# Kernel optimization log

Hardware: AMD Instinct MI355X
Metric: run time of the kernel (lower is better)

## Reference

```python
import jax, jax.numpy as jnp
import numpy as np

B, N, M = 2, 2048, 1024
C, CTX, H = 1024, 1024, 16
D = C // H
HID = int(C * 4.0)
EPS = 1e-6


def _ln(h):
    # LayerNorm32: fp32 layernorm, eps=1e-6, no affine params
    h32 = h.astype(jnp.float32)
    mu = jnp.mean(h32, axis=-1, keepdims=True)
    var = jnp.var(h32, axis=-1, keepdims=True)
    return ((h32 - mu) * jax.lax.rsqrt(var + EPS)).astype(h.dtype)


def _sdpa(q, k, v):
    # q: [B,Q,H,D], k/v: [B,K,H,D]
    scale = 1.0 / np.sqrt(D)
    s = jnp.einsum('bqhd,bkhd->bhqk', q, k) * scale
    p = jax.nn.softmax(s, axis=-1)
    return jnp.einsum('bhqk,bkhd->bqhd', p, v)


def _forward(x, context, Wqkv, bqkv, Wos, bos, Wq, bq, Wkv, bkv, Woc, boc, W1, b1, W2, b2):
    Bx, Nx, _ = x.shape
    Mx = context.shape[1]
    # --- self-attention (attn_mode='full') ---
    h = _ln(x)
    qkv = (h @ Wqkv + bqkv).reshape(Bx, Nx, 3, H, D)
    q, k, v = qkv[:, :, 0], qkv[:, :, 1], qkv[:, :, 2]
    a = _sdpa(q, k, v).reshape(Bx, Nx, C)
    x = x + (a @ Wos + bos)
    # --- cross-attention (always 'full') ---
    h = _ln(x)
    q = (h @ Wq + bq).reshape(Bx, Nx, H, D)
    kv = (context @ Wkv + bkv).reshape(Bx, Mx, 2, H, D)
    k, v = kv[:, :, 0], kv[:, :, 1]
    a = _sdpa(q, k, v).reshape(Bx, Nx, C)
    x = x + (a @ Woc + boc)
    # --- FFN with tanh-approx GELU ---
    h = _ln(x)
    x = x + (jax.nn.gelu(h @ W1 + b1, approximate=True) @ W2 + b2)
    return x


def setup_inputs() -> dict:
    key = jax.random.key(0)
    ks = jax.random.split(key, 12)
    rn = lambda k, shape: (jax.random.normal(k, shape, jnp.float32) * 0.02)
    return {
        'x': jax.random.normal(ks[0], (B, N, C), jnp.float32),
        'context': jax.random.normal(ks[1], (B, M, CTX), jnp.float32),
        'Wqkv': rn(ks[2], (C, 3 * C)), 'bqkv': jnp.zeros((3 * C,), jnp.float32),
        'Wos': rn(ks[3], (C, C)), 'bos': jnp.zeros((C,), jnp.float32),
        'Wq': rn(ks[4], (C, C)), 'bq': jnp.zeros((C,), jnp.float32),
        'Wkv': rn(ks[5], (CTX, 2 * C)), 'bkv': jnp.zeros((2 * C,), jnp.float32),
        'Woc': rn(ks[6], (C, C)), 'boc': jnp.zeros((C,), jnp.float32),
        'W1': rn(ks[7], (C, HID)), 'b1': jnp.zeros((HID,), jnp.float32),
        'W2': rn(ks[8], (HID, C)), 'b2': jnp.zeros((C,), jnp.float32),
    }


def reference(x, context, Wqkv, bqkv, Wos, bos, Wq, bq, Wkv, bkv, Woc, boc, W1, b1, W2, b2):
    return _forward(x, context, Wqkv, bqkv, Wos, bos, Wq, bq, Wkv, bkv, Woc, boc, W1, b1, W2, b2)
```

## Files before the change

### kernel.cpp

```cpp
#include <hip/hip_runtime.h>
#include <cstdint>

typedef unsigned short u16;
typedef short bf16x8 __attribute__((ext_vector_type(8)));
typedef unsigned short u16x8 __attribute__((ext_vector_type(8)));
typedef float f32x4 __attribute__((ext_vector_type(4)));

__device__ __forceinline__ u16 f2bf(float f) {
  union { float f; uint32_t u; } v; v.f = f;
  uint32_t r = (v.u + 0x7fffu + ((v.u >> 16) & 1u)) >> 16;
  return (u16)r;
}

__device__ __forceinline__ void gload_lds16(const u16* g, u16* l) {
  __builtin_amdgcn_global_load_lds(
      (const __attribute__((address_space(1))) void*)g,
      (__attribute__((address_space(3))) void*)l, 16, 0, 0);
}

__device__ __forceinline__ void ln_body(const float* __restrict__ x,
                                        u16* __restrict__ h, int row) {
  const int tid = threadIdx.x;
  const float4 v = *reinterpret_cast<const float4*>(x + (long)row * 1024 + tid * 4);
  float s  = v.x + v.y + v.z + v.w;
  float ss = v.x * v.x + v.y * v.y + v.z * v.z + v.w * v.w;
#pragma unroll
  for (int off = 32; off >= 1; off >>= 1) {
    s  += __shfl_xor(s, off, 64);
    ss += __shfl_xor(ss, off, 64);
  }
  __shared__ float red[8];
  const int wave = tid >> 6, lane = tid & 63;
  if (lane == 0) { red[wave] = s; red[4 + wave] = ss; }
  __syncthreads();
  s  = red[0] + red[1] + red[2] + red[3];
  ss = red[4] + red[5] + red[6] + red[7];
  const float mu   = s * (1.0f / 1024.0f);
  const float var  = ss * (1.0f / 1024.0f) - mu * mu;
  const float rstd = rsqrtf(var + 1e-6f);
  ushort4 o;
  o.x = f2bf((v.x - mu) * rstd);
  o.y = f2bf((v.y - mu) * rstd);
  o.z = f2bf((v.z - mu) * rstd);
  o.w = f2bf((v.w - mu) * rstd);
  *reinterpret_cast<ushort4*>(h + (long)row * 1024 + tid * 4) = o;
}

__global__ __launch_bounds__(256) void ln_kernel(const float* __restrict__ x,
                                                 u16* __restrict__ h) {
  ln_body(x, h, blockIdx.x);
}

struct WEnt { const float* W; u16* Wt; int K, N, tEnd; };
struct WEnts { WEnt e[4]; int n; };

__device__ __forceinline__ void wconv_body(const WEnts& args, int t) {
  __shared__ u16 tile[64][72];
  int i = 0, tStart = 0;
  while (i < args.n - 1 && t >= args.e[i].tEnd) { tStart = args.e[i].tEnd; i++; }
  const float* W = args.e[i].W;
  u16* Wt = args.e[i].Wt;
  const int K = args.e[i].K, N = args.e[i].N;
  const int rel = t - tStart;
  const int ntn = N >> 6;
  const int tn = rel % ntn, tk = rel / ntn;
  const int n0 = tn * 64, k0 = tk * 64;

  const int th = threadIdx.x;
  const int c4 = (th & 15) * 4;
  const int r  = th >> 4;
#pragma unroll
  for (int ii = 0; ii < 4; ii++) {
    const int row = ii * 16 + r;
    const float4 v = *reinterpret_cast<const float4*>(W + (long)(k0 + row) * N + n0 + c4);
    tile[c4 + 0][row] = f2bf(v.x);
    tile[c4 + 1][row] = f2bf(v.y);
    tile[c4 + 2][row] = f2bf(v.z);
    tile[c4 + 3][row] = f2bf(v.w);
  }
  __syncthreads();
  const int c8 = (th & 7) * 8;
  const int rn = th >> 3;
#pragma unroll
  for (int ii = 0; ii < 2; ii++) {
    const int row = ii * 32 + rn;
    *reinterpret_cast<u16x8*>(Wt + (long)(n0 + row) * K + k0 + c8) =
        *reinterpret_cast<const u16x8*>(&tile[row][c8]);
  }
}

__global__ __launch_bounds__(256) void wconvert_all(WEnts args) {
  wconv_body(args, blockIdx.x);
}

__global__ __launch_bounds__(256) void ln_wconv_combo(const float* __restrict__ x,
                                                      u16* __restrict__ h, int nLn,
                                                      WEnts args) {
  if ((int)blockIdx.x < nLn) ln_body(x, h, blockIdx.x);
  else                       wconv_body(args, blockIdx.x - nLn);
}

__global__ __launch_bounds__(256) void wconv_f2bf_combo(WEnts args, int nW,
                                                        const float* __restrict__ in,
                                                        u16* __restrict__ out) {
  if ((int)blockIdx.x < nW) {
    wconv_body(args, blockIdx.x);
  } else {
    const long i = ((long)(blockIdx.x - nW) * 256 + threadIdx.x) * 4;
    const float4 v = *reinterpret_cast<const float4*>(in + i);
    ushort4 o;
    o.x = f2bf(v.x); o.y = f2bf(v.y); o.z = f2bf(v.z); o.w = f2bf(v.w);
    *reinterpret_cast<ushort4*>(out + i) = o;
  }
}

__global__ __launch_bounds__(256) void vtrans(const u16* __restrict__ V,
                                              u16* __restrict__ Vt,
                                              int vStride, long vBatch, int nk) {
  __shared__ u16 tile[64][72];
  const int t = threadIdx.x;
  const int b = blockIdx.z, h = blockIdx.y, n0 = blockIdx.x * 64;
  const u16* vp = V + (long)b * vBatch + h * 64;
  u16* op = Vt + (long)(b * 16 + h) * 64 * (long)nk + n0;
  const int ch = t & 7;
#pragma unroll
  for (int i = 0; i < 2; i++) {
    const int n = (t >> 3) + i * 32;
    const u16x8 v = *reinterpret_cast<const u16x8*>(vp + (long)(n0 + n) * vStride + ch * 8);
#pragma unroll
    for (int j = 0; j < 8; j++) tile[ch * 8 + j][n] = v[j];
  }
  __syncthreads();
#pragma unroll
  for (int i = 0; i < 2; i++) {
    const int d = (t >> 3) + i * 32;
    *reinterpret_cast<u16x8*>(op + (long)d * nk + ch * 8) =
        *reinterpret_cast<const u16x8*>(&tile[d][ch * 8]);
  }
}

template <int TN, bool OUT_BF16, bool GELU_ACT, bool RES>
__device__ __forceinline__ void gemm_core(
    const u16* __restrict__ A, const u16* __restrict__ Bt,
    const float* __restrict__ bias, const float* __restrict__ res,
    void* __restrict__ Cout, int Ndim, int Kdim, int m0, int n0,
    u16* Al, u16* Bl, int qcols, float qscale) {
  constexpr int NF = TN / 32;
  constexpr int ABUF = 128 * 64;
  constexpr int BBUF = TN * 64;
  const int tid  = threadIdx.x;
  const int lane = tid & 63, wave = tid >> 6;
  const int quad = lane >> 4, l15 = lane & 15;
  const int wr = wave >> 1, wc = wave & 1;

  f32x4 acc[4][NF];
  const f32x4 vzero = {0.f, 0.f, 0.f, 0.f};
#pragma unroll
  for (int i = 0; i < 4; i++)
#pragma unroll
    for (int jj = 0; jj < NF; jj++) acc[i][jj] = vzero;

  const int srcRow = lane >> 3;
  const int srcG   = ((lane & 7) ^ (srcRow & 7)) * 8;
  const u16* gA = A  + (long)(m0 + srcRow) * Kdim + srcG;
  const u16* gB = Bt + (long)(n0 + srcRow) * Kdim + srcG;

  auto stage = [&](int k0, int p) {
#pragma unroll
    for (int i = 0; i < 4; i++)
      gload_lds16(gA + (long)(wave * 32 + i * 8) * Kdim + k0,
                  Al + p * ABUF + wave * 2048 + i * 512);
#pragma unroll
    for (int i = 0; i < TN / 32; i++)
      gload_lds16(gB + (long)(wave * (TN / 4) + i * 8) * Kdim + k0,
                  Bl + p * BBUF + wave * (TN * 16) + i * 512);
  };

  const int off0 = (quad ^ (l15 & 7)) * 8;

  stage(0, 0);
  int p = 0;
  for (int k0 = 0; k0 < Kdim; k0 += 64, p ^= 1) {
    __syncthreads();
    bf16x8 af[2][4], bfr[2][NF];
    const u16* ab = Al + p * ABUF;
    const u16* bb = Bl + p * BBUF;
#pragma unroll
    for (int mt = 0; mt < 4; mt++) {
      const int r = (wr * 64 + mt * 16 + l15) * 64;
      af[0][mt] = *reinterpret_cast<const bf16x8*>(ab + r + off0);
      af[1][mt] = *reinterpret_cast<const bf16x8*>(ab + r + (off0 ^ 32));
    }
#pragma unroll
    for (int nt = 0; nt < NF; nt++) {
      const int r = (wc * (NF * 16) + nt * 16 + l15) * 64;
      bfr[0][nt] = *reinterpret_cast<const bf16x8*>(bb + r + off0);
      bfr[1][nt] = *reinterpret_cast<const bf16x8*>(bb + r + (off0 ^ 32));
    }
    if (k0 + 64 < Kdim) stage(k0 + 64, p ^ 1);
#pragma unroll
    for (int s = 0; s < 2; s++)
#pragma unroll
      for (int mt = 0; mt < 4; mt++)
#pragma unroll
        for (int nt = 0; nt < NF; nt++)
          acc[mt][nt] = __builtin_amdgcn_mfma_f32_16x16x32_bf16(af[s][mt], bfr[s][nt], acc[mt][nt], 0, 0, 0);
  }

#pragma unroll
  for (int nt = 0; nt < NF; nt++) {
    const int col = n0 + wc * (NF * 16) + nt * 16 + l15;
    const float bv = bias[col];
    const float cs = (col < qcols) ? qscale : 1.0f;
#pragma unroll
    for (int mt = 0; mt < 4; mt++) {
#pragma unroll
      for (int r = 0; r < 4; r++) {
        const int row = m0 + wr * 64 + mt * 16 + quad * 4 + r;
        float y = (acc[mt][nt][r] + bv) * cs;
        if (GELU_ACT) {
          const float t = 0.7978845608028654f * (y + 0.044715f * y * y * y);
          y = y / (1.0f + __builtin_amdgcn_exp2f(-2.885390081777927f * t));
        }
        if (RES) y += res[(long)row * Ndim + col];
        if (OUT_BF16)
          ((u16*)Cout)[(long)row * Ndim + col] = f2bf(y);
        else
          ((float*)Cout)[(long)row * Ndim + col] = y;
      }
    }
  }
}

template <int TN, int SX, bool OUT_BF16, bool GELU_ACT, bool RES>
__global__ __launch_bounds__(256, 2) void gemm_bt(
    const u16* __restrict__ A, const u16* __restrict__ Bt,
    const float* __restrict__ bias, const float* __restrict__ res,
    void* __restrict__ Cout, int Ndim, int Kdim, int lx, int ly,
    int qcols, float qscale) {
  __shared__ u16 Al[2 * 128 * 64];
  __shared__ u16 Bl[2 * TN * 64];
  const int j = blockIdx.x;
  const int c = j & 7, kk = j >> 3;
  const int cx = c % SX, cy = c / SX;
  const int bx = cx * lx + (kk % lx);
  const int by = cy * ly + (kk / lx);
  gemm_core<TN, OUT_BF16, GELU_ACT, RES>(
      A, Bt, bias, res, Cout, Ndim, Kdim, by * 128, bx * TN, Al, Bl, qcols, qscale);
}

struct GemmSeg {
  const u16* A; const u16* Bt; const float* bias; u16* C;
  int Ndim, Kdim, SX, lx, ly, qcols; float qscale;
};
struct GemmDualP { GemmSeg s0, s1; int nBlk0; };

template <int TN>
__global__ __launch_bounds__(256, 2) void gemm_dual(GemmDualP pp) {
  __shared__ u16 Al[2 * 128 * 64];
  __shared__ u16 Bl[2 * TN * 64];
  int j = blockIdx.x;
  GemmSeg s;
  if (j < pp.nBlk0) { s = pp.s0; } else { s = pp.s1; j -= pp.nBlk0; }
  const int c = j & 7, kk = j >> 3;
  const int cx = c % s.SX, cy = c / s.SX;
  const int bx = cx * s.lx + (kk % s.lx);
  const int by = cy * s.ly + (kk / s.lx);
  gemm_core<TN, true, false, false>(
      s.A, s.Bt, s.bias, nullptr, s.C, s.Ndim, s.Kdim, by * 128, bx * TN, Al, Bl,
      s.qcols, s.qscale);
}

__global__ __launch_bounds__(256, 2) void attn_kernel(
    const u16* __restrict__ Q, const u16* __restrict__ K, const u16* __restrict__ Vt,
    u16* __restrict__ O, int nk, int qStride, int kStride, int oStride,
    long qBatch, long kBatch, long oBatch) {
  __shared__ u16 Kt[2][2 * 64 * 64];
  __shared__ u16 Vl[2][2 * 64 * 64];
  __shared__ u16 Pl[4][32 * 64];

  const int tid = threadIdx.x;
  const int lane = tid & 63, wave = tid >> 6;
  const int quad = lane >> 4, l15 = lane & 15;

  const int j = blockIdx.x;
  const int xcd = j & 7, slot = j >> 3;
  const int g = xcd * 4 + (slot >> 4);
  const int qt = slot & 15;
  const int hh = g & 15, b = g >> 4;

  const u16* qp = Q + (long)b * qBatch + hh * 64;
  const u16* kp = K + (long)b * kBatch + hh * 64;
  const u16* vp = Vt + (long)(b * 16 + hh) * 64 * (long)nk;

  bf16x8 qf[2][2];
  const int qrow = qt * 128 + wave * 32 + l15;
#pragma unroll
  for (int qg = 0; qg < 2; qg++) {
    qf[qg][0] = *reinterpret_cast<const bf16x8*>(qp + (long)(qrow + qg * 16) * qStride + quad * 8);
    qf[qg][1] = *reinterpret_cast<const bf16x8*>(qp + (long)(qrow + qg * 16) * qStride + 32 + quad * 8);
  }

  const int r8 = lane >> 3;
  const int gcol = ((lane & 7) ^ r8) * 8;
  const u16* kgA = kp + (long)(wave * 8 + r8) * kStride + gcol;
  const u16* kgB = kp + (long)((wave + 4) * 8 + r8) * kStride + gcol;
  const u16* vgA = vp + (long)(wave * 8 + r8) * nk + gcol;
  const u16* vgB = vp + (long)((wave + 4) * 8 + r8) * nk + gcol;

  const int cF = (quad ^ (l15 & 7)) * 8;

  const f32x4 vzero = {0.f, 0.f, 0.f, 0.f};
  const bf16x8 vones = {16256, 16256, 16256, 16256, 16256, 16256, 16256, 16256};
  f32x4 oAcc[2][4];
  f32x4 lAcc[2];
#pragma unroll
  for (int qg = 0; qg < 2; qg++) {
    lAcc[qg] = vzero;
#pragma unroll
    for (int i = 0; i < 4; i++) oAcc[qg][i] = vzero;
  }

  const int nWin = nk >> 7;
  const long kAdv = (long)128 * kStride;

  auto stage = [&](int w, int p) {
#pragma unroll
    for (int h2 = 0; h2 < 2; h2++) {
      const long kOff = w * kAdv + (long)(h2 * 64) * kStride;
      gload_lds16(kgA + kOff, &Kt[p][h2 * 4096 + wave * 512]);
      gload_lds16(kgB + kOff, &Kt[p][h2 * 4096 + (wave + 4) * 512]);
      const int vOff = w * 128 + h2 * 64;
      gload_lds16(vgA + vOff, &Vl[p][h2 * 4096 + wave * 512]);
      gload_lds16(vgB + vOff, &Vl[p][h2 * 4096 + (wave + 4) * 512]);
    }
  };

  stage(0, 0);
  int p = 0;
  for (int w = 0; w < nWin; w++, p ^= 1) {
    __syncthreads();
    if (w + 1 < nWin) stage(w + 1, p ^ 1);

#pragma unroll
    for (int h2 = 0; h2 < 2; h2++) {
      const u16* Kh = &Kt[p][h2 * 4096];
      const u16* Vh = &Vl[p][h2 * 4096];

      f32x4 st[2][4];
      __builtin_amdgcn_s_setprio(1);
#pragma unroll
      for (int mt = 0; mt < 4; mt++) {
        const bf16x8 kf0 = *reinterpret_cast<const bf16x8*>(&Kh[(mt * 16 + l15) * 64 + cF]);
        const bf16x8 kf1 = *reinterpret_cast<const bf16x8*>(&Kh[(mt * 16 + l15) * 64 + (cF ^ 32)]);
#pragma unroll
        for (int qg = 0; qg < 2; qg++) {
          f32x4 z = vzero;
          z = __builtin_amdgcn_mfma_f32_16x16x32_bf16(kf0, qf[qg][0], z, 0, 0, 0);
          z = __builtin_amdgcn_mfma_f32_16x16x32_bf16(kf1, qf[qg][1], z, 0, 0, 0);
          st[qg][mt] = z;
        }
      }
      __builtin_amdgcn_s_setprio(0);

#pragma unroll
      for (int qg = 0; qg < 2; qg++) {
        u16* plw = &Pl[wave][(qg * 16 + l15) * 64];
#pragma unroll
        for (int mt = 0; mt < 4; mt++) {
          const float e0 = __builtin_amdgcn_exp2f(st[qg][mt][0]);
          const float e1 = __builtin_amdgcn_exp2f(st[qg][mt][1]);
          const float e2 = __builtin_amdgcn_exp2f(st[qg][mt][2]);
          const float e3 = __builtin_amdgcn_exp2f(st[qg][mt][3]);
          uint2 w2;
          asm("v_cvt_pk_bf16_f32 %0, %1, %2" : "=v"(w2.x) : "v"(e0), "v"(e1));
          asm("v_cvt_pk_bf16_f32 %0, %1, %2" : "=v"(w2.y) : "v"(e2), "v"(e3));
          const int pcol = (((mt * 2 + (quad >> 1)) ^ (l15 & 7)) * 8) + (quad & 1) * 4;
          *reinterpret_cast<uint2*>(&plw[pcol]) = w2;
        }
      }

      bf16x8 pf[2][2];
#pragma unroll
      for (int qg = 0; qg < 2; qg++) {
        const u16* plw = &Pl[wave][(qg * 16 + l15) * 64];
        pf[qg][0] = *reinterpret_cast<const bf16x8*>(&plw[cF]);
        pf[qg][1] = *reinterpret_cast<const bf16x8*>(&plw[cF ^ 32]);
        lAcc[qg] = __builtin_amdgcn_mfma_f32_16x16x32_bf16(pf[qg][0], vones, lAcc[qg], 0, 0, 0);
        lAcc[qg] = __builtin_amdgcn_mfma_f32_16x16x32_bf16(pf[qg][1], vones, lAcc[qg], 0, 0, 0);
      }
      __builtin_amdgcn_s_setprio(1);
#pragma unroll
      for (int dt = 0; dt < 4; dt++) {
        const bf16x8 vf0 = *reinterpret_cast<const bf16x8*>(&Vh[(dt * 16 + l15) * 64 + cF]);
        const bf16x8 vf1 = *reinterpret_cast<const bf16x8*>(&Vh[(dt * 16 + l15) * 64 + (cF ^ 32)]);
#pragma unroll
        for (int qg = 0; qg < 2; qg++) {
          oAcc[qg][dt] = __builtin_amdgcn_mfma_f32_16x16x32_bf16(pf[qg][0], vf0, oAcc[qg][dt], 0, 0, 0);
          oAcc[qg][dt] = __builtin_amdgcn_mfma_f32_16x16x32_bf16(pf[qg][1], vf1, oAcc[qg][dt], 0, 0, 0);
        }
      }
      __builtin_amdgcn_s_setprio(0);
    }
  }

  u16* op = O + (long)b * oBatch + hh * 64;
#pragma unroll
  for (int qg = 0; qg < 2; qg++) {
    float lR[4];
#pragma unroll
    for (int r = 0; r < 4; r++) lR[r] = 1.0f / lAcc[qg][r];
#pragma unroll
    for (int dt = 0; dt < 4; dt++)
#pragma unroll
      for (int r = 0; r < 4; r++) {
        const int row = qt * 128 + wave * 32 + qg * 16 + quad * 4 + r;
        op[(long)row * oStride + dt * 16 + l15] = f2bf(oAcc[qg][dt][r] * lR[r]);
      }
  }
}

extern "C" void kernel_launch(void* const* d_in, const int* in_sizes, int n_in,
                              void* d_out, int out_size, void* d_ws, size_t ws_size,
                              hipStream_t stream) {
  const float* x    = (const float*)d_in[0];
  const float* ctx  = (const float*)d_in[1];
  const float* Wqkv = (const float*)d_in[2];
  const float* bqkv = (const float*)d_in[3];
  const float* Wos  = (const float*)d_in[4];
  const float* bos  = (const float*)d_in[5];
  const float* Wq   = (const float*)d_in[6];
  const float* bq   = (const float*)d_in[7];
  const float* Wkv  = (const float*)d_in[8];
  const float* bkv  = (const float*)d_in[9];
  const float* Woc  = (const float*)d_in[10];
  const float* boc  = (const float*)d_in[11];
  const float* W1   = (const float*)d_in[12];
  const float* b1   = (const float*)d_in[13];
  const float* W2   = (const float*)d_in[14];
  const float* b2   = (const float*)d_in[15];
  float* out = (float*)d_out;
  char* ws = (char*)d_ws;
  const size_t MB = 1024 * 1024;
  const float SCL = 0.18033688f;

  u16* h      = (u16*)ws;
  u16* abuf   = (u16*)(ws + 8 * MB);
  u16* wbuf   = (u16*)(ws + 8 * MB);
  u16* qkv    = (u16*)(ws + 16 * MB);
  u16* Wqkvt  = (u16*)(ws + 40 * MB);
  u16* Wost   = (u16*)(ws + 16 * MB);
  u16* Wqt    = (u16*)(ws + 18 * MB);
  u16* Wkvt   = (u16*)(ws + 20 * MB);
  u16* Woct   = (u16*)(ws + 24 * MB);
  u16* q2     = (u16*)(ws + 26 * MB);
  u16* kv2    = (u16*)(ws + 34 * MB);
  u16* ctxbf  = (u16*)(ws + 42 * MB);
  u16* VtCr   = (u16*)(ws + 16 * MB);
  u16* hid    = (u16*)(ws + 16 * MB);
  u16* VtSelf = h;
  u16* W1t    = wbuf;
  const bool bigWs = (ws_size >= 56 * MB);
  u16* W2t    = bigWs ? (u16*)(ws + 48 * MB) : wbuf;

  WEnts w1; w1.n = 1;

  w1.e[0] = {Wqkv, Wqkvt, 1024, 3072, 768};
  ln_wconv_combo<<<dim3(4096 + 768), dim3(256), 0, stream>>>(x, h, 4096, w1);
  gemm_bt<64, 2, true, false, false><<<dim3(1536), dim3(256), 0, stream>>>(
      h, Wqkvt, bqkv, nullptr, qkv, 3072, 1024, 24, 8, 1024, SCL);
  vtrans<<<dim3(32, 16, 2), dim3(256), 0, stream>>>(
      qkv + 2048, VtSelf, 3072, (long)2048 * 3072, 2048);
  attn_kernel<<<dim3(512), dim3(256), 0, stream>>>(
      qkv, qkv + 1024, VtSelf, abuf, 2048, 3072, 3072, 1024,
      (long)2048 * 3072, (long)2048 * 3072, (long)2048 * 1024);

  WEnts w4; w4.n = 4;
  w4.e[0] = {Wos, Wost, 1024, 1024, 256};
  w4.e[1] = {Wq,  Wqt,  1024, 1024, 512};
  w4.e[2] = {Wkv, Wkvt, 1024, 2048, 1024};
  w4.e[3] = {Woc, Woct, 1024, 1024, 1280};
  wconv_f2bf_combo<<<dim3(1280 + 2048), dim3(256), 0, stream>>>(w4, 1280, ctx, ctxbf);

  gemm_bt<64, 1, false, false, true><<<dim3(512), dim3(256), 0, stream>>>(
      abuf, Wost, bos, x, out, 1024, 1024, 16, 4, 0, 1.0f);
  ln_kernel<<<dim3(4096), dim3(256), 0, stream>>>(out, h);

  GemmDualP dp;
  dp.s0 = {h,     Wqt,  bq,  q2,  1024, 1024, 1, 16, 4, 1024, SCL};
  dp.s1 = {ctxbf, Wkvt, bkv, kv2, 2048, 1024, 2, 16, 4, 0, 1.0f};
  dp.nBlk0 = 512;
  gemm_dual<64><<<dim3(1024), dim3(256), 0, stream>>>(dp);
  vtrans<<<dim3(16, 16, 2), dim3(256), 0, stream>>>(
      kv2 + 1024, VtCr, 2048, (long)1024 * 2048, 1024);
  attn_kernel<<<dim3(512), dim3(256), 0, stream>>>(
      q2, kv2, VtCr, abuf, 1024, 1024, 2048, 1024,
      (long)2048 * 1024, (long)1024 * 2048, (long)2048 * 1024);
  gemm_bt<64, 1, false, false, true><<<dim3(512), dim3(256), 0, stream>>>(
      abuf, Woct, boc, out, out, 1024, 1024, 16, 4, 0, 1.0f);

  if (bigWs) {
    WEnts w2c; w2c.n = 2;
    w2c.e[0] = {W1, W1t, 1024, 4096, 1024};
    w2c.e[1] = {W2, W2t, 4096, 1024, 2048};
    ln_wconv_combo<<<dim3(4096 + 2048), dim3(256), 0, stream>>>(out, h, 4096, w2c);
    gemm_bt<128, 2, true, true, false><<<dim3(1024), dim3(256), 0, stream>>>(
        h, W1t, b1, nullptr, hid, 4096, 1024, 16, 8, 0, 1.0f);
  } else {
    w1.e[0] = {W1, W1t, 1024, 4096, 1024};
    ln_wconv_combo<<<dim3(4096 + 1024), dim3(256), 0, stream>>>(out, h, 4096, w1);
    gemm_bt<128, 2, true, true, false><<<dim3(1024), dim3(256), 0, stream>>>(
        h, W1t, b1, nullptr, hid, 4096, 1024, 16, 8, 0, 1.0f);
    w1.e[0] = {W2, W2t, 4096, 1024, 1024};
    wconvert_all<<<dim3(1024), dim3(256), 0, stream>>>(w1);
  }
  gemm_bt<64, 1, false, false, true><<<dim3(512), dim3(256), 0, stream>>>(
      hid, W2t, b2, out, out, 1024, 4096, 16, 4, 0, 1.0f);
}
```

Before: 419.8 us.

## Use intra-block split-K GEMM for FFN down-projection

Replaces the final FFN W2 GEMM (K=4096) with a new kernel that uses 64x64 output tiles and 1024 blocks, where each of the four waves handles a quarter of K with its own double-buffered LDS staging and no block-level barriers in the main loop. Partial accumulators are reduced through LDS at the end, then bias and residual are added. The intent is more parallelism and less barrier overhead for this long-K GEMM, at the cost of an LDS reduction step and smaller per-wave tiles.

```diff
diff --git a/kernel.cpp b/kernel.cpp
--- a/kernel.cpp
+++ b/kernel.cpp
@@ -269,6 +269,117 @@
   gemm_core<TN, true, false, false>(
       s.A, s.Bt, s.bias, nullptr, s.C, s.Ndim, s.Kdim, by * 128, bx * TN, Al, Bl,
       s.qcols, s.qscale);
+}
+
+__global__ __launch_bounds__(256, 2) void gemm_wsk(
+    const u16* __restrict__ A, const u16* __restrict__ Bt,
+    const float* __restrict__ bias, const float* __restrict__ res,
+    float* __restrict__ Cout, int Ndim, int Kdim) {
+  __shared__ u16 lds[2 * 4 * 2 * 2048];
+  u16* Albase = lds;
+  u16* Blbase = lds + 4 * 2 * 2048;
+
+  const int tid = threadIdx.x;
+  const int lane = tid & 63, wave = tid >> 6;
+  const int quad = lane >> 4, l15 = lane & 15;
+
+  const int j = blockIdx.x;
+  const int c = j & 7, kk = j >> 3;
+  const int bx = (c & 1) * 8 + (kk & 7);
+  const int by = (c >> 1) * 16 + (kk >> 3);
+  const int m0 = by * 64, n0 = bx * 64;
+
+  f32x4 acc[4][4];
+  const f32x4 vzero = {0.f, 0.f, 0.f, 0.f};
+#pragma unroll
+  for (int i = 0; i < 4; i++)
+#pragma unroll
+    for (int jj = 0; jj < 4; jj++) acc[i][jj] = vzero;
+
+  const int kbase = wave * (Kdim >> 2);
+  const long rowOff = (long)(lane >> 2) * Kdim + (((lane & 3) ^ ((lane >> 3) & 3)) * 8);
+  const u16* gA = A  + (long)m0 * Kdim + rowOff + kbase;
+  const u16* gB = Bt + (long)n0 * Kdim + rowOff + kbase;
+  u16* Aw = Albase + wave * 4096;
+  u16* Bw = Blbase + wave * 4096;
+
+  auto stageW = [&](int s, int p) {
+    const int k0 = s * 32;
+#pragma unroll
+    for (int cc = 0; cc < 4; cc++) {
+      gload_lds16(gA + (long)(cc * 16) * Kdim + k0, Aw + p * 2048 + cc * 512);
+      gload_lds16(gB + (long)(cc * 16) * Kdim + k0, Bw + p * 2048 + cc * 512);
+    }
+  };
+
+  const int swz = (quad ^ ((l15 >> 1) & 3)) * 8;
+  const int nSteps = Kdim >> 7;
+
+  stageW(0, 0);
+  stageW(1, 1);
+  int p = 0;
+  for (int s = 0; s < nSteps - 1; s++, p ^= 1) {
+    asm volatile("s_waitcnt vmcnt(8)" ::: "memory");
+    bf16x8 af[4], bf[4];
+#pragma unroll
+    for (int mt = 0; mt < 4; mt++)
+      af[mt] = *reinterpret_cast<const bf16x8*>(Aw + p * 2048 + (mt * 16 + l15) * 32 + swz);
+#pragma unroll
+    for (int nt = 0; nt < 4; nt++)
+      bf[nt] = *reinterpret_cast<const bf16x8*>(Bw + p * 2048 + (nt * 16 + l15) * 32 + swz);
+#pragma unroll
+    for (int mt = 0; mt < 4; mt++)
+#pragma unroll
+      for (int nt = 0; nt < 4; nt++)
+        acc[mt][nt] = __builtin_amdgcn_mfma_f32_16x16x32_bf16(af[mt], bf[nt], acc[mt][nt], 0, 0, 0);
+    if (s < nSteps - 2) stageW(s + 2, p);
+  }
+  asm volatile("s_waitcnt vmcnt(0)" ::: "memory");
+  {
+    bf16x8 af[4], bf[4];
+#pragma unroll
+    for (int mt = 0; mt < 4; mt++)
+      af[mt] = *reinterpret_cast<const bf16x8*>(Aw + p * 2048 + (mt * 16 + l15) * 32 + swz);
+#pragma unroll
+    for (int nt = 0; nt < 4; nt++)
+      bf[nt] = *reinterpret_cast<const bf16x8*>(Bw + p * 2048 + (nt * 16 + l15) * 32 + swz);
+#pragma unroll
+    for (int mt = 0; mt < 4; mt++)
+#pragma unroll
+      for (int nt = 0; nt < 4; nt++)
+        acc[mt][nt] = __builtin_amdgcn_mfma_f32_16x16x32_bf16(af[mt], bf[nt], acc[mt][nt], 0, 0, 0);
+  }
+
+  __syncthreads();
+  float* lf = reinterpret_cast<float*>(lds);
+  float* myreg = lf + wave * 4096;
+#pragma unroll
+  for (int mt = 0; mt < 4; mt++)
+#pragma unroll
+    for (int nt = 0; nt < 4; nt++)
+      *reinterpret_cast<f32x4*>(myreg + lane * 64 + mt * 16 + nt * 4) = acc[mt][nt];
+  __syncthreads();
+
+  const int Lq  = lane >> 2;
+  const int mtR = lane & 3;
+  f32x4 sum[4] = {vzero, vzero, vzero, vzero};
+#pragma unroll
+  for (int rg = 0; rg < 4; rg++) {
+    const float* rp = lf + rg * 4096 + (wave * 16 + Lq) * 64 + mtR * 16;
+#pragma unroll
+    for (int nt = 0; nt < 4; nt++)
+      sum[nt] += *reinterpret_cast<const f32x4*>(rp + nt * 4);
+  }
+#pragma unroll
+  for (int nt = 0; nt < 4; nt++) {
+    const int col = n0 + nt * 16 + Lq;
+    const float bv = bias[col];
+#pragma unroll
+    for (int r = 0; r < 4; r++) {
+      const int row = m0 + mtR * 16 + wave * 4 + r;
+      Cout[(long)row * Ndim + col] = sum[nt][r] + bv + res[(long)row * Ndim + col];
+    }
+  }
 }
 
 __global__ __launch_bounds__(256, 2) void attn_kernel(
@@ -514,6 +625,6 @@
     w1.e[0] = {W2, W2t, 4096, 1024, 1024};
     wconvert_all<<<dim3(1024), dim3(256), 0, stream>>>(w1);
   }
-  gemm_bt<64, 1, false, false, true><<<dim3(512), dim3(256), 0, stream>>>(
-      hid, W2t, b2, out, out, 1024, 4096, 16, 4, 0, 1.0f);
-}
+  gemm_wsk<<<dim3(1024), dim3(256), 0, stream>>>(
+      hid, W2t, b2, out, out, 1024, 4096);
+}
```

Measured after the change: 449.9 us. +7.2%, slower.
